# Performance work log

Measured on AMD Instinct MI355X. Metric: run time of the kernel, lower is better.

Reference implementation:

```python
import jax, jax.numpy as jnp
import numpy as np

E = 8        # n_routed_experts
K = 4        # num_experts_per_tok
T = 1024     # tokens
H = 1024     # hidden_size
I = 1408     # moe_intermediate_size


def setup_inputs() -> dict:
    key = jax.random.key(0)
    ks = jax.random.split(key, 6)
    hidden_states = jax.random.normal(ks[0], (T, H), jnp.float32)
    rw = jax.random.uniform(ks[1], (T, K), jnp.float32)
    router_weights = rw / jnp.sum(rw, axis=-1, keepdims=True)  # normalized top-k router weights
    selected_experts = jax.random.randint(ks[2], (T, K), 0, E, jnp.int32)
    gate_w = jax.random.normal(ks[3], (E, H, I), jnp.float32) * (H ** -0.5)  # lecun_normal-ish
    up_w = jax.random.normal(ks[4], (E, H, I), jnp.float32) * (H ** -0.5)
    down_w = jax.random.normal(ks[5], (E, I, H), jnp.float32) * (I ** -0.5)
    return {
        'hidden_states': hidden_states,
        'router_weights': router_weights,
        'gate_w': gate_w,
        'up_w': up_w,
        'down_w': down_w,
        'selected_experts': selected_experts,
    }


def _grouped_matmul(x, w, seg):
    # x: [m, k] tokens sorted by expert; w: [E, k, n]; seg: [m] expert id per row.
    # Grouped GEMM expressed as E masked GEMMs (fixed small loop over experts);
    # a custom kernel would do true variable-group-size grouped GEMM.
    out = jnp.zeros((x.shape[0], w.shape[-1]), x.dtype)
    for e in range(w.shape[0]):
        out = out + jnp.where((seg == e)[:, None], x, jnp.zeros((), x.dtype)) @ w[e]
    return out


def reference(hidden_states, router_weights, gate_w, up_w, down_w, selected_experts):
    t, k = selected_experts.shape
    flat = selected_experts.ravel()                       # [t*k]
    hs = jnp.repeat(hidden_states, k, axis=0)             # [t*k, H]
    sort_idx = jnp.argsort(flat)                          # dispatch: sort tokens by expert
    seg = flat[sort_idx]
    xs = hs[sort_idx]
    gate = _grouped_matmul(xs, gate_w, seg)               # [t*k, I]
    up = _grouped_matmul(xs, up_w, seg)                   # [t*k, I]
    h = jax.nn.silu(gate) * up                            # fused SwiGLU
    down = _grouped_matmul(h, down_w, seg)                # [t*k, H]
    unsort = jnp.argsort(sort_idx)                        # scatter back to token order
    out = down[unsort].reshape(t, k, -1)
    return jnp.sum(out * router_weights[..., None], axis=1)  # weighted combine [t, H]
```

## Files before the change

kernel.cpp:

```cpp
#include <hip/hip_runtime.h>
#include <hip/hip_bf16.h>
#include <cstdint>
#include <cstddef>

#define NE 8
#define NT 1024
#define NK 4
#define NH 1024
#define NI 1408
#define NA (NT * NK)
#define BM 128
#define MAXTILES 40
#define PADSLOTS 5120

typedef short short8 __attribute__((ext_vector_type(8)));
typedef float f32x4 __attribute__((ext_vector_type(4)));
typedef unsigned short u16;

#define WS_HDR   0
#define WS_SORT  1024
#define WS_XBF   21504
#define WS_GT    2118656
#define WS_UT    25187328
#define WS_DT    48256000
#define WS_HB    71324672
#define WS_DTMP  85742592

__device__ __forceinline__ u16 f2b(float f) {
  union { float f; uint32_t u; } c; c.f = f;
  uint32_t u = c.u;
  return (u16)((u + 0x7FFFu + ((u >> 16) & 1u)) >> 16);
}

__device__ __forceinline__ void llds16(const void* g, void* l) {
  __builtin_amdgcn_global_load_lds(
      (const __attribute__((address_space(1))) void*)g,
      (__attribute__((address_space(3))) void*)l, 16, 0, 0);
}

__global__ void bucket_kernel(const int* __restrict__ sel, int* __restrict__ hdr,
                              int* __restrict__ sorted) {
  __shared__ int cnt[NE], fill[NE], poff_s[NE + 1];
  int tid = threadIdx.x;
  if (tid < NE) { cnt[tid] = 0; fill[tid] = 0; }
  __syncthreads();
  for (int i = tid; i < NA; i += 256) atomicAdd(&cnt[sel[i]], 1);
  __syncthreads();
  if (tid == 0) {
    int off = 0, nt = 0;
    for (int e = 0; e < NE; ++e) {
      poff_s[e] = off;
      int tiles = (cnt[e] + BM - 1) / BM;
      for (int j = 0; j < tiles; ++j) { hdr[32 + nt] = e; hdr[80 + nt] = off + j * BM; ++nt; }
      off += tiles * BM;
    }
    poff_s[NE] = off;
    hdr[17] = nt;
    for (int e = 0; e < NE; ++e) hdr[e] = cnt[e];
    for (int e = 0; e <= NE; ++e) hdr[8 + e] = poff_s[e];
  }
  __syncthreads();
  for (int i = tid; i < PADSLOTS; i += 256) sorted[i] = -1;
  __syncthreads();
  for (int i = tid; i < NA; i += 256) {
    int e = sel[i];
    int p = atomicAdd(&fill[e], 1);
    sorted[poff_s[e] + p] = i;
  }
}

__global__ void cvt_x_kernel(const float* __restrict__ src, u16* __restrict__ dst) {
  int i = (blockIdx.x * 256 + threadIdx.x) * 4;
  float4 v = *(const float4*)&src[i];
  ushort4 o;
  o.x = f2b(v.x); o.y = f2b(v.y); o.z = f2b(v.z); o.w = f2b(v.w);
  *(ushort4*)&dst[i] = o;
}

__global__ __launch_bounds__(256) void transcvt_all(
    const float* __restrict__ gw, const float* __restrict__ uw, const float* __restrict__ dw,
    u16* __restrict__ gT, u16* __restrict__ uT, u16* __restrict__ dT) {
  __shared__ float t[64][65];
  int z = blockIdx.z;
  int tensor = z >> 3, e = z & 7;
  const float* src; u16* dst; int K, N, kb, nb;
  if (tensor == 0)      { src = gw; dst = gT; }
  else if (tensor == 1) { src = uw; dst = uT; }
  else                  { src = dw; dst = dT; }
  if (tensor < 2) { K = NH; N = NI; nb = blockIdx.x; kb = blockIdx.y; }
  else            { K = NI; N = NH; kb = blockIdx.x; nb = blockIdx.y; }
  int k0 = kb * 64, n0 = nb * 64;
  src += (size_t)e * K * N;
  dst += (size_t)e * K * N;
  int tid = threadIdx.x;
  for (int i = 0; i < 4; ++i) {
    int idx = i * 256 + tid;
    int r = idx >> 4, c = idx & 15;
    *(float4*)&t[r][c * 4] = *(const float4*)&src[(size_t)(k0 + r) * N + n0 + c * 4];
  }
  __syncthreads();
  for (int i = 0; i < 2; ++i) {
    int idx = i * 256 + tid;
    int n = idx >> 3, kc = idx & 7;
    u16 o[8];
#pragma unroll
    for (int j = 0; j < 8; ++j) o[j] = f2b(t[kc * 8 + j][n]);
    *(short8*)&dst[(size_t)(n0 + n) * K + k0 + kc * 8] = *(const short8*)o;
  }
}

__global__ __launch_bounds__(256, 2) void gemm1_kernel(
    const u16* __restrict__ xbf, const u16* __restrict__ gT, const u16* __restrict__ uT,
    u16* __restrict__ hbuf, const int* __restrict__ hdr, const int* __restrict__ sorted) {
  int tile = blockIdx.x;
  if (tile >= hdr[17]) return;
  int e = hdr[32 + tile];
  int slot0 = hdr[80 + tile];
  int n0 = blockIdx.y * 64;
  int tid = threadIdx.x;

  __shared__ u16 sA[128 * 64];
  __shared__ u16 sBg[64 * 64];
  __shared__ u16 sBu[64 * 64];

  const u16* aptr[4];
  for (int s = 0; s < 4; ++s) {
    int idx = s * 256 + tid;
    int row = idx >> 3, c = idx & 7;
    int kc = c ^ (row & 7);
    int as = sorted[slot0 + row];
    int trow = (as >= 0) ? (as >> 2) : 0;
    aptr[s] = xbf + (size_t)trow * NH + kc * 8;
  }
  const u16 *bgp[2], *bup[2];
  for (int s = 0; s < 2; ++s) {
    int idx = s * 256 + tid;
    int n = idx >> 3, c = idx & 7;
    int kc = c ^ (n & 7);
    size_t o = ((size_t)e * NI + n0 + n) * NH + kc * 8;
    bgp[s] = gT + o; bup[s] = uT + o;
  }

  int lane = tid & 63, wave = tid >> 6;
  int wm = wave >> 1, wn = wave & 1;
  int l15 = lane & 15, quad = lane >> 4;
  int sw = l15 & 7;

  f32x4 accg[4][2] = {}; f32x4 accu[4][2] = {};

  for (int kt = 0; kt < NH / 64; ++kt) {
    int ko = kt * 64;
    for (int s = 0; s < 4; ++s) llds16(aptr[s] + ko, &sA[(s * 256 + tid) * 8]);
    for (int s = 0; s < 2; ++s) {
      llds16(bgp[s] + ko, &sBg[(s * 256 + tid) * 8]);
      llds16(bup[s] + ko, &sBu[(s * 256 + tid) * 8]);
    }
    __syncthreads();
    for (int ks = 0; ks < 2; ++ks) {
      int pos = ((ks * 4 + quad) ^ sw) * 8;
      short8 av[4], bg[2], bu[2];
      for (int mf = 0; mf < 4; ++mf)
        av[mf] = *(const short8*)&sA[(wm * 64 + mf * 16 + l15) * 64 + pos];
      for (int nf = 0; nf < 2; ++nf) {
        bg[nf] = *(const short8*)&sBg[(wn * 32 + nf * 16 + l15) * 64 + pos];
        bu[nf] = *(const short8*)&sBu[(wn * 32 + nf * 16 + l15) * 64 + pos];
      }
      for (int mf = 0; mf < 4; ++mf)
        for (int nf = 0; nf < 2; ++nf) {
          accg[mf][nf] = __builtin_amdgcn_mfma_f32_16x16x32_bf16(av[mf], bg[nf], accg[mf][nf], 0, 0, 0);
          accu[mf][nf] = __builtin_amdgcn_mfma_f32_16x16x32_bf16(av[mf], bu[nf], accu[mf][nf], 0, 0, 0);
        }
    }
    __syncthreads();
  }

  for (int mf = 0; mf < 4; ++mf)
    for (int nf = 0; nf < 2; ++nf)
      for (int r = 0; r < 4; ++r) {
        int row = wm * 64 + mf * 16 + quad * 4 + r;
        int col = n0 + wn * 32 + nf * 16 + l15;
        float g = accg[mf][nf][r], u = accu[mf][nf][r];
        float hv = (g / (1.f + __expf(-g))) * u;
        hbuf[(size_t)(slot0 + row) * NI + col] = f2b(hv);
      }
}

__global__ __launch_bounds__(256, 2) void gemm2_kernel(
    const u16* __restrict__ hbuf, const u16* __restrict__ dT,
    float* __restrict__ dtmp, const int* __restrict__ hdr, const int* __restrict__ sorted) {
  int tile = blockIdx.x;
  if (tile >= hdr[17]) return;
  int e = hdr[32 + tile];
  int slot0 = hdr[80 + tile];
  int n0 = blockIdx.y * 128;
  int tid = threadIdx.x;

  __shared__ u16 sA[128 * 64];
  __shared__ u16 sB[128 * 64];

  const u16 *ap[4], *bp[4];
  for (int s = 0; s < 4; ++s) {
    int idx = s * 256 + tid;
    int r = idx >> 3, c = idx & 7;
    int kc = c ^ (r & 7);
    ap[s] = hbuf + (size_t)(slot0 + r) * NI + kc * 8;
    bp[s] = dT + ((size_t)e * NH + n0 + r) * NI + kc * 8;
  }

  int lane = tid & 63, wave = tid >> 6;
  int wm = wave >> 1, wn = wave & 1;
  int l15 = lane & 15, quad = lane >> 4;
  int sw = l15 & 7;

  f32x4 acc[4][4] = {};

  for (int kt = 0; kt < NI / 64; ++kt) {
    int ko = kt * 64;
    for (int s = 0; s < 4; ++s) llds16(ap[s] + ko, &sA[(s * 256 + tid) * 8]);
    for (int s = 0; s < 4; ++s) llds16(bp[s] + ko, &sB[(s * 256 + tid) * 8]);
    __syncthreads();
    for (int ks = 0; ks < 2; ++ks) {
      int pos = ((ks * 4 + quad) ^ sw) * 8;
      short8 av[4], bv[4];
      for (int mf = 0; mf < 4; ++mf)
        av[mf] = *(const short8*)&sA[(wm * 64 + mf * 16 + l15) * 64 + pos];
      for (int nf = 0; nf < 4; ++nf)
        bv[nf] = *(const short8*)&sB[(wn * 64 + nf * 16 + l15) * 64 + pos];
      for (int mf = 0; mf < 4; ++mf)
        for (int nf = 0; nf < 4; ++nf)
          acc[mf][nf] = __builtin_amdgcn_mfma_f32_16x16x32_bf16(av[mf], bv[nf], acc[mf][nf], 0, 0, 0);
    }
    __syncthreads();
  }

  for (int mf = 0; mf < 4; ++mf) {
    int rowb = wm * 64 + mf * 16 + quad * 4;
    for (int r = 0; r < 4; ++r) {
      int as = sorted[slot0 + rowb + r];
      if (as < 0) continue;
      float* orow = dtmp + (size_t)as * NH + n0 + wn * 64;
      for (int nf = 0; nf < 4; ++nf)
        orow[nf * 16 + l15] = acc[mf][nf][r];
    }
  }
}

__global__ void combine_kernel(const float* __restrict__ dtmp, const float* __restrict__ rw,
                               float* __restrict__ out) {
  int t = blockIdx.x;
  int c = threadIdx.x * 4;
  float4 acc = make_float4(0.f, 0.f, 0.f, 0.f);
  for (int k = 0; k < NK; ++k) {
    float w = rw[t * NK + k];
    float4 v = *(const float4*)&dtmp[(size_t)(t * NK + k) * NH + c];
    acc.x += w * v.x; acc.y += w * v.y; acc.z += w * v.z; acc.w += w * v.w;
  }
  *(float4*)&out[(size_t)t * NH + c] = acc;
}

extern "C" void kernel_launch(void* const* d_in, const int* in_sizes, int n_in,
                              void* d_out, int out_size, void* d_ws, size_t ws_size,
                              hipStream_t stream) {
  const float* hs  = (const float*)d_in[0];
  const float* rw  = (const float*)d_in[1];
  const float* gw  = (const float*)d_in[2];
  const float* uw  = (const float*)d_in[3];
  const float* dw  = (const float*)d_in[4];
  const int*   sel = (const int*)d_in[5];
  float* out = (float*)d_out;

  char* ws = (char*)d_ws;
  int*  hdr    = (int*)(ws + WS_HDR);
  int*  sorted = (int*)(ws + WS_SORT);
  u16*  xbf    = (u16*)(ws + WS_XBF);
  u16*  gT     = (u16*)(ws + WS_GT);
  u16*  uT     = (u16*)(ws + WS_UT);
  u16*  dT     = (u16*)(ws + WS_DT);
  u16*  hb     = (u16*)(ws + WS_HB);
  float* dtmp  = (float*)(ws + WS_DTMP);

  hipLaunchKernelGGL(bucket_kernel, dim3(1), dim3(256), 0, stream, sel, hdr, sorted);
  hipLaunchKernelGGL(cvt_x_kernel, dim3(NT * NH / 1024), dim3(256), 0, stream, hs, xbf);
  hipLaunchKernelGGL(transcvt_all, dim3(22, 16, 24), dim3(256), 0, stream, gw, uw, dw, gT, uT, dT);
  hipLaunchKernelGGL(gemm1_kernel, dim3(MAXTILES, NI / 64), dim3(256), 0, stream, xbf, gT, uT, hb, hdr, sorted);
  hipLaunchKernelGGL(gemm2_kernel, dim3(MAXTILES, NH / 128), dim3(256), 0, stream, hb, dT, dtmp, hdr, sorted);
  hipLaunchKernelGGL(combine_kernel, dim3(NT), dim3(256), 0, stream, dtmp, rw, out);
}
```

Baseline: 261.0 us.

## Fuse x conversion into weight transpose kernel, widen tiles, raise GEMM occupancy

Folds the hidden-state bf16 conversion into the weight transpose-convert kernel as an extra grid row, which removes one launch. Each transpose block now covers a 64x128 tile, converts to bf16 before staging in shared memory (halving LDS use), and reads through nontemporal loads. The GEMM kernels' launch bounds are raised to 4 blocks per SM, which may force register spills. The weight conversion is memory-bound, so cheaper staging and streaming loads aim to cut that dominant cost.

```diff
diff --git a/kernel.cpp b/kernel.cpp
--- a/kernel.cpp
+++ b/kernel.cpp
@@ -15,6 +15,7 @@
 
 typedef short short8 __attribute__((ext_vector_type(8)));
 typedef float f32x4 __attribute__((ext_vector_type(4)));
+typedef float f4v __attribute__((ext_vector_type(4)));
 typedef unsigned short u16;
 
 #define WS_HDR   0
@@ -69,47 +70,64 @@
   }
 }
 
-__global__ void cvt_x_kernel(const float* __restrict__ src, u16* __restrict__ dst) {
-  int i = (blockIdx.x * 256 + threadIdx.x) * 4;
-  float4 v = *(const float4*)&src[i];
-  ushort4 o;
-  o.x = f2b(v.x); o.y = f2b(v.y); o.z = f2b(v.z); o.w = f2b(v.w);
-  *(ushort4*)&dst[i] = o;
-}
-
 __global__ __launch_bounds__(256) void transcvt_all(
     const float* __restrict__ gw, const float* __restrict__ uw, const float* __restrict__ dw,
-    u16* __restrict__ gT, u16* __restrict__ uT, u16* __restrict__ dT) {
-  __shared__ float t[64][65];
-  int z = blockIdx.z;
-  int tensor = z >> 3, e = z & 7;
+    const float* __restrict__ hs,
+    u16* __restrict__ gT, u16* __restrict__ uT, u16* __restrict__ dT, u16* __restrict__ xbf) {
+  int tid = threadIdx.x;
+  int y = blockIdx.y;
+  if (y == 24) {
+    for (int i = blockIdx.x * 256 + tid; i * 4 < NT * NH; i += 176 * 256) {
+      f4v v = __builtin_nontemporal_load((const f4v*)&hs[i * 4]);
+      ushort4 o;
+      o.x = f2b(v.x); o.y = f2b(v.y); o.z = f2b(v.z); o.w = f2b(v.w);
+      *(ushort4*)&xbf[i * 4] = o;
+    }
+    return;
+  }
+  __shared__ u16 t2[2][64][72];
+  int tensor = y >> 3, e = y & 7;
   const float* src; u16* dst; int K, N, kb, nb;
   if (tensor == 0)      { src = gw; dst = gT; }
   else if (tensor == 1) { src = uw; dst = uT; }
   else                  { src = dw; dst = dT; }
-  if (tensor < 2) { K = NH; N = NI; nb = blockIdx.x; kb = blockIdx.y; }
-  else            { K = NI; N = NH; kb = blockIdx.x; nb = blockIdx.y; }
-  int k0 = kb * 64, n0 = nb * 64;
+  if (tensor < 2) { K = NH; N = NI; nb = blockIdx.x % 11; kb = blockIdx.x / 11; }
+  else            { K = NI; N = NH; nb = blockIdx.x % 8;  kb = blockIdx.x / 8;  }
+  int k0 = kb * 64, n0 = nb * 128;
   src += (size_t)e * K * N;
   dst += (size_t)e * K * N;
-  int tid = threadIdx.x;
-  for (int i = 0; i < 4; ++i) {
-    int idx = i * 256 + tid;
-    int r = idx >> 4, c = idx & 15;
-    *(float4*)&t[r][c * 4] = *(const float4*)&src[(size_t)(k0 + r) * N + n0 + c * 4];
-  }
-  __syncthreads();
-  for (int i = 0; i < 2; ++i) {
-    int idx = i * 256 + tid;
-    int n = idx >> 3, kc = idx & 7;
-    u16 o[8];
-#pragma unroll
-    for (int j = 0; j < 8; ++j) o[j] = f2b(t[kc * 8 + j][n]);
-    *(short8*)&dst[(size_t)(n0 + n) * K + k0 + kc * 8] = *(const short8*)o;
-  }
-}
-
-__global__ __launch_bounds__(256, 2) void gemm1_kernel(
+
+  int r = tid >> 4, c = tid & 15;
+  f4v v[2][4];
+#pragma unroll
+  for (int t = 0; t < 2; ++t)
+#pragma unroll
+    for (int i = 0; i < 4; ++i)
+      v[t][i] = __builtin_nontemporal_load(
+          (const f4v*)&src[(size_t)(k0 + r + 16 * i) * N + n0 + t * 64 + c * 4]);
+#pragma unroll
+  for (int t = 0; t < 2; ++t)
+#pragma unroll
+    for (int i = 0; i < 4; ++i) {
+      ushort4 o;
+      o.x = f2b(v[t][i].x); o.y = f2b(v[t][i].y); o.z = f2b(v[t][i].z); o.w = f2b(v[t][i].w);
+      *(ushort4*)&t2[t][r + 16 * i][c * 4] = o;
+    }
+  __syncthreads();
+#pragma unroll
+  for (int t = 0; t < 2; ++t)
+#pragma unroll
+    for (int i = 0; i < 2; ++i) {
+      int idx = i * 256 + tid;
+      int n = idx >> 3, kc = idx & 7;
+      u16 o[8];
+#pragma unroll
+      for (int j = 0; j < 8; ++j) o[j] = t2[t][kc * 8 + j][n];
+      *(short8*)&dst[(size_t)(n0 + t * 64 + n) * K + k0 + kc * 8] = *(const short8*)o;
+    }
+}
+
+__global__ __launch_bounds__(256, 4) void gemm1_kernel(
     const u16* __restrict__ xbf, const u16* __restrict__ gT, const u16* __restrict__ uT,
     u16* __restrict__ hbuf, const int* __restrict__ hdr, const int* __restrict__ sorted) {
   int tile = blockIdx.x;
@@ -185,7 +203,7 @@
       }
 }
 
-__global__ __launch_bounds__(256, 2) void gemm2_kernel(
+__global__ __launch_bounds__(256, 4) void gemm2_kernel(
     const u16* __restrict__ hbuf, const u16* __restrict__ dT,
     float* __restrict__ dtmp, const int* __restrict__ hdr, const int* __restrict__ sorted) {
   int tile = blockIdx.x;
@@ -280,8 +298,8 @@
   float* dtmp  = (float*)(ws + WS_DTMP);
 
   hipLaunchKernelGGL(bucket_kernel, dim3(1), dim3(256), 0, stream, sel, hdr, sorted);
-  hipLaunchKernelGGL(cvt_x_kernel, dim3(NT * NH / 1024), dim3(256), 0, stream, hs, xbf);
-  hipLaunchKernelGGL(transcvt_all, dim3(22, 16, 24), dim3(256), 0, stream, gw, uw, dw, gT, uT, dT);
+  hipLaunchKernelGGL(transcvt_all, dim3(176, 25), dim3(256), 0, stream,
+                     gw, uw, dw, hs, gT, uT, dT, xbf);
   hipLaunchKernelGGL(gemm1_kernel, dim3(MAXTILES, NI / 64), dim3(256), 0, stream, xbf, gT, uT, hb, hdr, sorted);
   hipLaunchKernelGGL(gemm2_kernel, dim3(MAXTILES, NH / 128), dim3(256), 0, stream, hb, dT, dtmp, hdr, sorted);
   hipLaunchKernelGGL(combine_kernel, dim3(NT), dim3(256), 0, stream, dtmp, rw, out);
```

Result: faster. 248.5 us (-4.8%).
